# Performance work log

Hardware: AMD Instinct MI355X
Metric: run time of the kernel (lower is better)

Reference implementation:

```python
import jax, jax.numpy as jnp
import numpy as np


def _mlp(x, w1, b1, w2, b2):
    # torch Mlp: fc1 -> GELU (exact erf) -> fc2, dropout off in eval
    h = jax.nn.gelu(x @ w1 + b1, approximate=False)
    return h @ w2 + b2


def _nearest(x, oh, ow):
    # torch F.interpolate mode='nearest' on [B,h,w,d]: src = floor(dst*in/out)
    h, w = x.shape[1], x.shape[2]
    ih = (np.arange(oh) * h) // oh
    iw = (np.arange(ow) * w) // ow
    return x[:, ih][:, :, iw]


def setup_inputs() -> dict:
    key = jax.random.key(0)
    ks = jax.random.split(key, 8)
    B, s0, dim, nPnt, new2 = 4, 12, 256, 128, 48  # new_size=24
    sc = 0.02
    return {
        "token_init": jax.random.normal(ks[0], (B, s0, s0, dim), jnp.float32),
        "point_token": jax.random.normal(ks[1], (B, nPnt, dim), jnp.float32),
        "nr_w1": jax.random.normal(ks[2], (nPnt, 4 * nPnt), jnp.float32) * sc,
        "nr_b1": jnp.zeros((4 * nPnt,), jnp.float32),
        "nr_w2": jax.random.normal(ks[3], (4 * nPnt, nPnt), jnp.float32) * sc,
        "nr_b2": jnp.zeros((nPnt,), jnp.float32),
        "na_w1": jax.random.normal(ks[4], (nPnt, 4 * nPnt), jnp.float32) * sc,
        "na_b1": jnp.zeros((4 * nPnt,), jnp.float32),
        "na_w2": jax.random.normal(ks[5], (4 * nPnt, nPnt), jnp.float32) * sc,
        "na_b2": jnp.zeros((nPnt,), jnp.float32),
        "tf_w1": jax.random.normal(ks[6], (new2, new2), jnp.float32) * sc,
        "tf_b1": jnp.zeros((new2,), jnp.float32),
        "tf_w2": jax.random.normal(ks[7], (new2, 1), jnp.float32) * sc,
        "tf_b2": jnp.zeros((1,), jnp.float32),
        "height": 120,
        "width": 160,
    }


def reference(token_init, point_token, nr_w1, nr_b1, nr_w2, nr_b2,
              na_w1, na_b1, na_w2, na_b2, tf_w1, tf_b1, tf_w2, tf_b2,
              height, width):
    B, nPnt, dim = point_token.shape
    new_size = tf_w1.shape[0] // 2
    scale = dim ** (-0.5)
    # is_init=False path: repeat_interleave x2 along H and W
    t = jnp.repeat(jnp.repeat(token_init, 2, axis=1), 2, axis=2)  # [B,2s,2s,d]
    token_raw = _nearest(t, height, width)                        # [B,H,W,d]
    t_exp = _nearest(t, new_size, new_size)                       # [B,sH,sW,d]
    sH = sW = new_size
    token_templ = t_exp.reshape(B, sH * sW, dim)
    node_adj = jnp.einsum('bnd,bpd->bnp', token_templ, point_token) * scale
    node_adj = _mlp(node_adj, nr_w1, nr_b1, nr_w2, nr_b2)
    node_adj = node_adj.reshape(B, sH, sW, nPnt)
    node_w = jnp.einsum('bhwp,bhwd->bhpd', node_adj, t_exp) * (sW ** -0.5)
    node_h = jnp.einsum('bhwp,bhwd->bwpd', node_adj, t_exp) * (sH ** -0.5)
    token_n = jnp.concatenate([node_w, node_h], axis=1)           # [B,2s,nPnt,d]
    x = token_n.reshape(B, sH + sW, nPnt * dim).transpose(0, 2, 1)  # [B,nPnt*d,2s]
    token_fused = _mlp(x, tf_w1, tf_b1, tf_w2, tf_b2)             # [B,nPnt*d,1]
    token_fused = token_fused.reshape(B, nPnt, dim)
    token_raw_f = token_raw.reshape(B, height * width, dim)
    node_attn = jnp.einsum('bnd,bpd->bnp', token_raw_f, point_token) * scale
    node_attn = jax.nn.softmax(_mlp(node_attn, na_w1, na_b1, na_w2, na_b2), axis=-1)
    token_new = node_attn @ token_fused + token_raw_f             # [B,HW,d]
    return token_new
```

## Files before the change

kernel.cpp:

```cpp
#include <hip/hip_runtime.h>
#include <math.h>

#define B     4
#define DIM   256
#define NP    128
#define NS    144
#define HID   512
#define NROW  576
#define H_OUT 120
#define W_OUT 160

__device__ __forceinline__ float gelu_exact(float x) {
    return 0.5f * x * (1.0f + erff(x * 0.70710678118654752440f));
}

__global__ __launch_bounds__(256) void k_q(
    const float* __restrict__ ti, const float* __restrict__ pt,
    float* __restrict__ Q)
{
    const int g0 = blockIdx.x * 2;
    const int b  = g0 / NS;
    const int t  = threadIdx.x;
    __shared__ float4 xs[2][64];
    __shared__ float  qp[2][2][NP];

    for (int i = t; i < 128; i += 256) {
        int r = i >> 6, c = i & 63;
        xs[r][c] = ((const float4*)ti)[(g0 + r) * 64 + c];
    }
    __syncthreads();

    const int p = t & 127, dh = t >> 7;
    const float4* pr = (const float4*)pt + (b * NP + p) * 64 + dh * 32;
    float a0 = 0.f, a1 = 0.f;
    #pragma unroll 8
    for (int i = 0; i < 32; ++i) {
        float4 v  = pr[i];
        float4 x0 = xs[0][dh * 32 + i];
        float4 x1 = xs[1][dh * 32 + i];
        a0 += v.x * x0.x + v.y * x0.y + v.z * x0.z + v.w * x0.w;
        a1 += v.x * x1.x + v.y * x1.y + v.z * x1.z + v.w * x1.w;
    }
    qp[dh][0][p] = a0;
    qp[dh][1][p] = a1;
    __syncthreads();

    const int r = t >> 7;
    Q[(g0 + r) * NP + p] = (qp[0][r][p] + qp[1][r][p]) * 0.0625f;
}

__global__ __launch_bounds__(256) void k_h(
    const float* __restrict__ Q,
    const float* __restrict__ nr_w1, const float* __restrict__ nr_b1,
    const float* __restrict__ na_w1, const float* __restrict__ na_b1,
    float* __restrict__ H)
{
    const int mlp = blockIdx.x / 288;
    const int t2  = blockIdx.x % 288;
    const int g0  = (t2 >> 2) * 8;
    const int kbase = (t2 & 3) * 128;
    const int t   = threadIdx.x;
    const float* __restrict__ w1 = mlp ? na_w1 : nr_w1;
    const float* __restrict__ b1 = mlp ? na_b1 : nr_b1;

    __shared__ float qs[8][NP];
    for (int i = t; i < 8 * NP; i += 256) {
        int r = i >> 7, p = i & 127;
        qs[r][p] = Q[(g0 + r) * NP + p];
    }
    __syncthreads();

    const int kq = t & 31;
    const int rg = t >> 5;
    const int k0 = kbase + kq * 4;

    float4 acc = *(const float4*)(b1 + k0);
    const float* __restrict__ wp = w1 + k0;
    #pragma unroll 8
    for (int p = 0; p < NP; ++p) {
        const float4 w4 = *(const float4*)(wp + p * HID);
        const float  qv = qs[rg][p];
        acc.x += qv * w4.x;
        acc.y += qv * w4.y;
        acc.z += qv * w4.z;
        acc.w += qv * w4.w;
    }
    float4 o;
    o.x = gelu_exact(acc.x);
    o.y = gelu_exact(acc.y);
    o.z = gelu_exact(acc.z);
    o.w = gelu_exact(acc.w);
    *(float4*)(H + (size_t)(mlp * NROW + g0 + rg) * HID + k0) = o;
}

__global__ __launch_bounds__(256) void k_l(
    const float* __restrict__ H,
    const float* __restrict__ nr_w2, const float* __restrict__ nr_b2,
    const float* __restrict__ na_w2, const float* __restrict__ na_b2,
    float* __restrict__ nadjT, float* __restrict__ attn)
{
    const int mlp = blockIdx.x / 288;
    const int g0  = (blockIdx.x % 288) * 2;
    const int b   = g0 / NS;
    const int n0  = g0 % NS;
    const int t   = threadIdx.x;
    const float* __restrict__ w2 = mlp ? na_w2 : nr_w2;
    const float* __restrict__ b2 = mlp ? na_b2 : nr_b2;

    __shared__ float hs[2][HID];
    {
        const int r = t >> 7, q = t & 127;
        ((float4*)hs[r])[q] =
            ((const float4*)H)[(size_t)(mlp * NROW + g0 + r) * 128 + q];
    }
    __syncthreads();

    const int pq = t & 31;
    const int kg = t >> 5;
    const float4* __restrict__ w24 = (const float4*)w2 + pq;

    float4 acc0 = make_float4(0.f, 0.f, 0.f, 0.f);
    float4 acc1 = make_float4(0.f, 0.f, 0.f, 0.f);
    #pragma unroll 8
    for (int i = 0; i < 64; ++i) {
        const int k = kg * 64 + i;
        const float4 w4 = w24[k * 32];
        const float h0 = hs[0][k];
        const float h1 = hs[1][k];
        acc0.x += h0 * w4.x; acc0.y += h0 * w4.y;
        acc0.z += h0 * w4.z; acc0.w += h0 * w4.w;
        acc1.x += h1 * w4.x; acc1.y += h1 * w4.y;
        acc1.z += h1 * w4.z; acc1.w += h1 * w4.w;
    }

    __shared__ float par[16][NP];
    ((float4*)par[kg * 2 + 0])[pq] = acc0;
    ((float4*)par[kg * 2 + 1])[pq] = acc1;
    __syncthreads();

    const int r = t >> 7, p = t & 127;
    float logit = b2[p];
    #pragma unroll
    for (int kg2 = 0; kg2 < 8; ++kg2) logit += par[kg2 * 2 + r][p];

    if (mlp == 0) {
        nadjT[(size_t)(b * NP + p) * NS + n0 + r] = logit;
    } else {
        __shared__ float red[2][NP];
        red[r][p] = logit;
        __syncthreads();
        for (int s = 64; s > 0; s >>= 1) {
            if (p < s) red[r][p] = fmaxf(red[r][p], red[r][p + s]);
            __syncthreads();
        }
        const float mx = red[r][0];
        __syncthreads();
        const float e = expf(logit - mx);
        red[r][p] = e;
        __syncthreads();
        for (int s = 64; s > 0; s >>= 1) {
            if (p < s) red[r][p] += red[r][p + s];
            __syncthreads();
        }
        attn[(g0 + r) * NP + p] = e / red[r][0];
    }
}

__global__ __launch_bounds__(256) void k_fold(
    const float* __restrict__ nadjT, const float* __restrict__ ti,
    const float* __restrict__ w1, const float* __restrict__ b1,
    const float* __restrict__ w2, const float* __restrict__ b2,
    float* __restrict__ tf)
{
    const int b = blockIdx.x >> 7;
    const int p = blockIdx.x & 127;
    const int t = threadIdx.x;
    __shared__ float an[NS];
    __shared__ float w1p[24][48];
    __shared__ float b1s[48];
    __shared__ float w2s[48];

    if (t < NS) an[t] = nadjT[(size_t)(b * NP + p) * NS + t];
    if (t >= 192 && t < 240) {
        int k = t - 192;
        b1s[k] = b1[k];
        w2s[k] = w2[k];
    }
    for (int i = t; i < 24 * 48; i += 256) {
        int m = i / 48, k = i - m * 48;
        w1p[m][k] = w1[(2 * m) * 48 + k] + w1[(2 * m + 1) * 48 + k];
    }
    __syncthreads();

    const int d = t;
    const float* __restrict__ tb = ti + (size_t)b * NS * DIM + d;
    float v[24];
    #pragma unroll
    for (int m = 0; m < 24; ++m) v[m] = 0.f;
    #pragma unroll
    for (int y = 0; y < 12; ++y) {
        #pragma unroll
        for (int x = 0; x < 12; ++x) {
            const int n = y * 12 + x;
            const float tv = tb[n * DIM];
            const float a  = an[n];
            v[y]      += a * tv;
            v[12 + x] += a * tv;
        }
    }
    const float c = 0.40824829046386301637f;
    #pragma unroll
    for (int m = 0; m < 24; ++m) v[m] *= c;

    float acc = b2[0];
    for (int k = 0; k < 48; ++k) {
        float tt = b1s[k];
        #pragma unroll
        for (int m = 0; m < 24; ++m) tt += v[m] * w1p[m][k];
        acc += gelu_exact(tt) * w2s[k];
    }
    tf[(size_t)(b * NP + p) * DIM + d] = acc;
}

__global__ __launch_bounds__(256) void k_final(
    const float* __restrict__ attn, const float* __restrict__ tf,
    const float* __restrict__ ti, float4* __restrict__ out)
{
    const int g = blockIdx.x;
    const int b = g / NS;
    const int n = g % NS;
    const int t = threadIdx.x;
    const int dq = t & 63;
    const int pg = t >> 6;

    __shared__ float  at[NP];
    __shared__ float4 par4[4][64];
    __shared__ float4 rowf[64];

    if (t < NP) at[t] = attn[g * NP + t];
    __syncthreads();

    const float4* __restrict__ tp = (const float4*)tf + (size_t)b * NP * 64 + dq;
    float4 acc = make_float4(0.f, 0.f, 0.f, 0.f);
    #pragma unroll 8
    for (int i = 0; i < 32; ++i) {
        const int p = pg * 32 + i;
        const float  a  = at[p];
        const float4 tv = tp[p * 64];
        acc.x += a * tv.x; acc.y += a * tv.y;
        acc.z += a * tv.z; acc.w += a * tv.w;
    }
    par4[pg][dq] = acc;
    __syncthreads();

    if (t < 64) {
        float4 s = par4[0][t];
        const float4 s1 = par4[1][t], s2 = par4[2][t], s3 = par4[3][t];
        const float4 tiv = ((const float4*)ti)[(size_t)g * 64 + t];
        s.x += s1.x + s2.x + s3.x + tiv.x;
        s.y += s1.y + s2.y + s3.y + tiv.y;
        s.z += s1.z + s2.z + s3.z + tiv.z;
        s.w += s1.w + s2.w + s3.w + tiv.w;
        rowf[t] = s;
    }
    __syncthreads();

    const int y = n / 12, x = n % 12;
    const int w_lo = (40 * x + 2) / 3;
    const int w_hi = (40 * x + 42) / 3;
    const float4 val = rowf[dq];
    for (int h = 10 * y; h < 10 * y + 10; ++h) {
        float4* orow = out + (size_t)((b * H_OUT + h) * W_OUT) * 64 + dq;
        for (int w = w_lo + pg; w < w_hi; w += 4) {
            orow[w * 64] = val;
        }
    }
}

extern "C" void kernel_launch(void* const* d_in, const int* in_sizes, int n_in,
                              void* d_out, int out_size, void* d_ws, size_t ws_size,
                              hipStream_t stream) {
    (void)in_sizes; (void)n_in; (void)out_size; (void)ws_size;
    const float* token_init  = (const float*)d_in[0];
    const float* point_token = (const float*)d_in[1];
    const float* nr_w1 = (const float*)d_in[2];
    const float* nr_b1 = (const float*)d_in[3];
    const float* nr_w2 = (const float*)d_in[4];
    const float* nr_b2 = (const float*)d_in[5];
    const float* na_w1 = (const float*)d_in[6];
    const float* na_b1 = (const float*)d_in[7];
    const float* na_w2 = (const float*)d_in[8];
    const float* na_b2 = (const float*)d_in[9];
    const float* tf_w1 = (const float*)d_in[10];
    const float* tf_b1 = (const float*)d_in[11];
    const float* tf_w2 = (const float*)d_in[12];
    const float* tf_b2 = (const float*)d_in[13];

    float* out = (float*)d_out;
    float* ws  = (float*)d_ws;
    float* Q      = ws;
    float* H      = Q + NROW * NP;
    float* nadjT  = H + 2 * NROW * HID;
    float* attn   = nadjT + NROW * NP;
    float* tf     = attn + NROW * NP;

    k_q<<<NROW / 2, 256, 0, stream>>>(token_init, point_token, Q);
    k_h<<<576, 256, 0, stream>>>(Q, nr_w1, nr_b1, na_w1, na_b1, H);
    k_l<<<576, 256, 0, stream>>>(H, nr_w2, nr_b2, na_w2, na_b2, nadjT, attn);
    k_fold<<<B * NP, 256, 0, stream>>>(nadjT, token_init,
                                       tf_w1, tf_b1, tf_w2, tf_b2, tf);
    k_final<<<NROW, 256, 0, stream>>>(attn, tf, token_init, (float4*)out);
}
```

Baseline: 176.5 us.

## Fuse Q projection and both MLP layers into one kernel per 4-row tile

Merges k_q, k_h and k_l into a single k_mlp kernel. Each block processes 4 token rows for one of the two MLPs and keeps Q and the hidden activations in shared memory, so the H buffer is no longer written to or read back from global memory. This also removes two kernel launches and raises weight reuse to 4 rows per load. In exchange the grid shrinks to 288 blocks, each doing more serial work with heavier shared-memory use, and Q is recomputed separately by each of the two MLPs. It also vectorizes the nadjT load in k_fold and adds size_t index casts.

```diff
diff --git a/kernel.cpp b/kernel.cpp
--- a/kernel.cpp
+++ b/kernel.cpp
@@ -14,155 +14,143 @@
     return 0.5f * x * (1.0f + erff(x * 0.70710678118654752440f));
 }
 
-__global__ __launch_bounds__(256) void k_q(
+__global__ __launch_bounds__(256) void k_mlp(
     const float* __restrict__ ti, const float* __restrict__ pt,
-    float* __restrict__ Q)
-{
-    const int g0 = blockIdx.x * 2;
-    const int b  = g0 / NS;
-    const int t  = threadIdx.x;
-    __shared__ float4 xs[2][64];
-    __shared__ float  qp[2][2][NP];
-
-    for (int i = t; i < 128; i += 256) {
-        int r = i >> 6, c = i & 63;
-        xs[r][c] = ((const float4*)ti)[(g0 + r) * 64 + c];
-    }
-    __syncthreads();
-
-    const int p = t & 127, dh = t >> 7;
-    const float4* pr = (const float4*)pt + (b * NP + p) * 64 + dh * 32;
-    float a0 = 0.f, a1 = 0.f;
-    #pragma unroll 8
-    for (int i = 0; i < 32; ++i) {
-        float4 v  = pr[i];
-        float4 x0 = xs[0][dh * 32 + i];
-        float4 x1 = xs[1][dh * 32 + i];
-        a0 += v.x * x0.x + v.y * x0.y + v.z * x0.z + v.w * x0.w;
-        a1 += v.x * x1.x + v.y * x1.y + v.z * x1.z + v.w * x1.w;
-    }
-    qp[dh][0][p] = a0;
-    qp[dh][1][p] = a1;
-    __syncthreads();
-
-    const int r = t >> 7;
-    Q[(g0 + r) * NP + p] = (qp[0][r][p] + qp[1][r][p]) * 0.0625f;
-}
-
-__global__ __launch_bounds__(256) void k_h(
-    const float* __restrict__ Q,
     const float* __restrict__ nr_w1, const float* __restrict__ nr_b1,
+    const float* __restrict__ nr_w2, const float* __restrict__ nr_b2,
     const float* __restrict__ na_w1, const float* __restrict__ na_b1,
-    float* __restrict__ H)
-{
-    const int mlp = blockIdx.x / 288;
-    const int t2  = blockIdx.x % 288;
-    const int g0  = (t2 >> 2) * 8;
-    const int kbase = (t2 & 3) * 128;
-    const int t   = threadIdx.x;
-    const float* __restrict__ w1 = mlp ? na_w1 : nr_w1;
-    const float* __restrict__ b1 = mlp ? na_b1 : nr_b1;
-
-    __shared__ float qs[8][NP];
-    for (int i = t; i < 8 * NP; i += 256) {
-        int r = i >> 7, p = i & 127;
-        qs[r][p] = Q[(g0 + r) * NP + p];
-    }
-    __syncthreads();
-
-    const int kq = t & 31;
-    const int rg = t >> 5;
-    const int k0 = kbase + kq * 4;
-
-    float4 acc = *(const float4*)(b1 + k0);
-    const float* __restrict__ wp = w1 + k0;
-    #pragma unroll 8
-    for (int p = 0; p < NP; ++p) {
-        const float4 w4 = *(const float4*)(wp + p * HID);
-        const float  qv = qs[rg][p];
-        acc.x += qv * w4.x;
-        acc.y += qv * w4.y;
-        acc.z += qv * w4.z;
-        acc.w += qv * w4.w;
-    }
-    float4 o;
-    o.x = gelu_exact(acc.x);
-    o.y = gelu_exact(acc.y);
-    o.z = gelu_exact(acc.z);
-    o.w = gelu_exact(acc.w);
-    *(float4*)(H + (size_t)(mlp * NROW + g0 + rg) * HID + k0) = o;
-}
-
-__global__ __launch_bounds__(256) void k_l(
-    const float* __restrict__ H,
-    const float* __restrict__ nr_w2, const float* __restrict__ nr_b2,
     const float* __restrict__ na_w2, const float* __restrict__ na_b2,
     float* __restrict__ nadjT, float* __restrict__ attn)
 {
-    const int mlp = blockIdx.x / 288;
-    const int g0  = (blockIdx.x % 288) * 2;
-    const int b   = g0 / NS;
-    const int n0  = g0 % NS;
-    const int t   = threadIdx.x;
+    const int mlp  = blockIdx.x / 144;
+    const int tile = blockIdx.x % 144;
+    const int g0 = tile * 4;
+    const int b  = g0 / NS;
+    const int n0 = g0 % NS;
+    const int t  = threadIdx.x;
+
+    const float* __restrict__ w1 = mlp ? na_w1 : nr_w1;
+    const float* __restrict__ b1 = mlp ? na_b1 : nr_b1;
     const float* __restrict__ w2 = mlp ? na_w2 : nr_w2;
     const float* __restrict__ b2 = mlp ? na_b2 : nr_b2;
 
-    __shared__ float hs[2][HID];
+    __shared__ float4 xs4[4][64];
+    __shared__ float  qs[4][NP];
+    __shared__ float  hs[4][HID];
+    __shared__ float  par[8][4][NP];
+    __shared__ float  red[4][NP];
+
     {
-        const int r = t >> 7, q = t & 127;
-        ((float4*)hs[r])[q] =
-            ((const float4*)H)[(size_t)(mlp * NROW + g0 + r) * 128 + q];
-    }
-    __syncthreads();
-
-    const int pq = t & 31;
-    const int kg = t >> 5;
-    const float4* __restrict__ w24 = (const float4*)w2 + pq;
-
-    float4 acc0 = make_float4(0.f, 0.f, 0.f, 0.f);
-    float4 acc1 = make_float4(0.f, 0.f, 0.f, 0.f);
-    #pragma unroll 8
-    for (int i = 0; i < 64; ++i) {
-        const int k = kg * 64 + i;
-        const float4 w4 = w24[k * 32];
-        const float h0 = hs[0][k];
-        const float h1 = hs[1][k];
-        acc0.x += h0 * w4.x; acc0.y += h0 * w4.y;
-        acc0.z += h0 * w4.z; acc0.w += h0 * w4.w;
-        acc1.x += h1 * w4.x; acc1.y += h1 * w4.y;
-        acc1.z += h1 * w4.z; acc1.w += h1 * w4.w;
-    }
-
-    __shared__ float par[16][NP];
-    ((float4*)par[kg * 2 + 0])[pq] = acc0;
-    ((float4*)par[kg * 2 + 1])[pq] = acc1;
-    __syncthreads();
-
-    const int r = t >> 7, p = t & 127;
-    float logit = b2[p];
+        const int r = t >> 6, c = t & 63;
+        xs4[r][c] = ((const float4*)ti)[(size_t)(g0 + r) * 64 + c];
+    }
+    __syncthreads();
+
+    const int p  = t & 127;
+    const int rh = t >> 7;
+    {
+        const float4* __restrict__ pr =
+            (const float4*)pt + (size_t)(b * NP + p) * 64;
+        float a0 = 0.f, a1 = 0.f;
+        #pragma unroll 8
+        for (int i = 0; i < 64; ++i) {
+            const float4 v  = pr[i];
+            const float4 x0 = xs4[rh][i];
+            const float4 x1 = xs4[rh + 2][i];
+            a0 += v.x*x0.x + v.y*x0.y + v.z*x0.z + v.w*x0.w;
+            a1 += v.x*x1.x + v.y*x1.y + v.z*x1.z + v.w*x1.w;
+        }
+        qs[rh][p]     = a0 * 0.0625f;
+        qs[rh + 2][p] = a1 * 0.0625f;
+    }
+    __syncthreads();
+
+    {
+        const int kq = t & 127;
+        const int k0 = kq * 4;
+        float4 acc0 = *(const float4*)(b1 + k0);
+        float4 acc1 = acc0;
+        const float* __restrict__ wp = w1 + k0;
+        #pragma unroll 8
+        for (int pp = 0; pp < NP; ++pp) {
+            const float4 w4 = *(const float4*)(wp + (size_t)pp * HID);
+            const float q0 = qs[rh][pp];
+            const float q1 = qs[rh + 2][pp];
+            acc0.x += q0*w4.x; acc0.y += q0*w4.y;
+            acc0.z += q0*w4.z; acc0.w += q0*w4.w;
+            acc1.x += q1*w4.x; acc1.y += q1*w4.y;
+            acc1.z += q1*w4.z; acc1.w += q1*w4.w;
+        }
+        float4 o0, o1;
+        o0.x = gelu_exact(acc0.x); o0.y = gelu_exact(acc0.y);
+        o0.z = gelu_exact(acc0.z); o0.w = gelu_exact(acc0.w);
+        o1.x = gelu_exact(acc1.x); o1.y = gelu_exact(acc1.y);
+        o1.z = gelu_exact(acc1.z); o1.w = gelu_exact(acc1.w);
+        ((float4*)hs[rh])[kq]     = o0;
+        ((float4*)hs[rh + 2])[kq] = o1;
+    }
+    __syncthreads();
+
+    {
+        const int pq = t & 31;
+        const int p0 = pq * 4;
+        const int kg = t >> 5;
+        float4 a0 = make_float4(0.f,0.f,0.f,0.f);
+        float4 a1 = a0, a2 = a0, a3 = a0;
+        const float4* __restrict__ w24 = (const float4*)(w2 + p0);
+        #pragma unroll 8
+        for (int i = 0; i < 64; ++i) {
+            const int k = kg * 64 + i;
+            const float4 w4 = w24[(size_t)k * 32];
+            const float h0 = hs[0][k], h1 = hs[1][k];
+            const float h2 = hs[2][k], h3 = hs[3][k];
+            a0.x += h0*w4.x; a0.y += h0*w4.y; a0.z += h0*w4.z; a0.w += h0*w4.w;
+            a1.x += h1*w4.x; a1.y += h1*w4.y; a1.z += h1*w4.z; a1.w += h1*w4.w;
+            a2.x += h2*w4.x; a2.y += h2*w4.y; a2.z += h2*w4.z; a2.w += h2*w4.w;
+            a3.x += h3*w4.x; a3.y += h3*w4.y; a3.z += h3*w4.z; a3.w += h3*w4.w;
+        }
+        ((float4*)par[kg][0])[pq] = a0;
+        ((float4*)par[kg][1])[pq] = a1;
+        ((float4*)par[kg][2])[pq] = a2;
+        ((float4*)par[kg][3])[pq] = a3;
+    }
+    __syncthreads();
+
+    float lg0 = b2[p], lg1 = lg0;
     #pragma unroll
-    for (int kg2 = 0; kg2 < 8; ++kg2) logit += par[kg2 * 2 + r][p];
+    for (int kg = 0; kg < 8; ++kg) {
+        lg0 += par[kg][rh][p];
+        lg1 += par[kg][rh + 2][p];
+    }
 
     if (mlp == 0) {
-        nadjT[(size_t)(b * NP + p) * NS + n0 + r] = logit;
+        float* __restrict__ dst = nadjT + (size_t)(b * NP + p) * NS + n0;
+        dst[rh]     = lg0;
+        dst[rh + 2] = lg1;
     } else {
-        __shared__ float red[2][NP];
-        red[r][p] = logit;
+        red[rh][p] = lg0; red[rh + 2][p] = lg1;
         __syncthreads();
         for (int s = 64; s > 0; s >>= 1) {
-            if (p < s) red[r][p] = fmaxf(red[r][p], red[r][p + s]);
+            if (p < s) {
+                red[rh][p]     = fmaxf(red[rh][p],     red[rh][p + s]);
+                red[rh + 2][p] = fmaxf(red[rh + 2][p], red[rh + 2][p + s]);
+            }
             __syncthreads();
         }
-        const float mx = red[r][0];
+        const float m0 = red[rh][0], m1 = red[rh + 2][0];
         __syncthreads();
-        const float e = expf(logit - mx);
-        red[r][p] = e;
+        const float e0 = expf(lg0 - m0), e1 = expf(lg1 - m1);
+        red[rh][p] = e0; red[rh + 2][p] = e1;
         __syncthreads();
         for (int s = 64; s > 0; s >>= 1) {
-            if (p < s) red[r][p] += red[r][p + s];
+            if (p < s) {
+                red[rh][p]     += red[rh][p + s];
+                red[rh + 2][p] += red[rh + 2][p + s];
+            }
             __syncthreads();
         }
-        attn[(g0 + r) * NP + p] = e / red[r][0];
+        attn[(size_t)(g0 + rh) * NP + p]     = e0 / red[rh][0];
+        attn[(size_t)(g0 + rh + 2) * NP + p] = e1 / red[rh + 2][0];
     }
 }
 
@@ -180,14 +168,17 @@
     __shared__ float b1s[48];
     __shared__ float w2s[48];
 
-    if (t < NS) an[t] = nadjT[(size_t)(b * NP + p) * NS + t];
+    if (t < 36) {
+        ((float4*)an)[t] =
+            ((const float4*)(nadjT + (size_t)(b * NP + p) * NS))[t];
+    }
     if (t >= 192 && t < 240) {
-        int k = t - 192;
+        const int k = t - 192;
         b1s[k] = b1[k];
         w2s[k] = w2[k];
     }
     for (int i = t; i < 24 * 48; i += 256) {
-        int m = i / 48, k = i - m * 48;
+        const int m = i / 48, k = i - m * 48;
         w1p[m][k] = w1[(2 * m) * 48 + k] + w1[(2 * m + 1) * 48 + k];
     }
     __syncthreads();
@@ -237,16 +228,16 @@
     __shared__ float4 par4[4][64];
     __shared__ float4 rowf[64];
 
-    if (t < NP) at[t] = attn[g * NP + t];
+    if (t < NP) at[t] = attn[(size_t)g * NP + t];
     __syncthreads();
 
     const float4* __restrict__ tp = (const float4*)tf + (size_t)b * NP * 64 + dq;
     float4 acc = make_float4(0.f, 0.f, 0.f, 0.f);
     #pragma unroll 8
     for (int i = 0; i < 32; ++i) {
-        const int p = pg * 32 + i;
-        const float  a  = at[p];
-        const float4 tv = tp[p * 64];
+        const int pp = pg * 32 + i;
+        const float  a  = at[pp];
+        const float4 tv = tp[(size_t)pp * 64];
         acc.x += a * tv.x; acc.y += a * tv.y;
         acc.z += a * tv.z; acc.w += a * tv.w;
     }
@@ -270,9 +261,9 @@
     const int w_hi = (40 * x + 42) / 3;
     const float4 val = rowf[dq];
     for (int h = 10 * y; h < 10 * y + 10; ++h) {
-        float4* orow = out + (size_t)((b * H_OUT + h) * W_OUT) * 64 + dq;
+        float4* __restrict__ orow = out + (size_t)((b * H_OUT + h) * W_OUT) * 64 + dq;
         for (int w = w_lo + pg; w < w_hi; w += 4) {
-            orow[w * 64] = val;
+            orow[(size_t)w * 64] = val;
         }
     }
 }
@@ -298,15 +289,14 @@
 
     float* out = (float*)d_out;
     float* ws  = (float*)d_ws;
-    float* Q      = ws;
-    float* H      = Q + NROW * NP;
-    float* nadjT  = H + 2 * NROW * HID;
-    float* attn   = nadjT + NROW * NP;
-    float* tf     = attn + NROW * NP;
-
-    k_q<<<NROW / 2, 256, 0, stream>>>(token_init, point_token, Q);
-    k_h<<<576, 256, 0, stream>>>(Q, nr_w1, nr_b1, na_w1, na_b1, H);
-    k_l<<<576, 256, 0, stream>>>(H, nr_w2, nr_b2, na_w2, na_b2, nadjT, attn);
+    float* nadjT = ws;
+    float* attn  = nadjT + NROW * NP;
+    float* tf    = attn + NROW * NP;
+
+    k_mlp<<<288, 256, 0, stream>>>(token_init, point_token,
+                                   nr_w1, nr_b1, nr_w2, nr_b2,
+                                   na_w1, na_b1, na_w2, na_b2,
+                                   nadjT, attn);
     k_fold<<<B * NP, 256, 0, stream>>>(nadjT, token_init,
                                        tf_w1, tf_b1, tf_w2, tf_b2, tf);
     k_final<<<NROW, 256, 0, stream>>>(attn, tf, token_init, (float4*)out);
```

Result: faster. 171.1 us (-3.1%).
